# Performance work log

Measured on AMD Instinct MI355X. Metric: run time of the kernel, lower is better.

The kernel has to match this reference:

```python
import jax, jax.numpy as jnp
import numpy as np

B, N, FEAT, HID = 1024, 128, 512, 256


def setup_inputs() -> dict:
    key = jax.random.key(0)
    k1, k2, k3, k4, k5, k6 = jax.random.split(key, 6)
    x = jax.random.normal(k1, (B, FEAT), dtype=jnp.float32)
    labels = jax.random.randint(k2, (B,), 0, N, dtype=jnp.int64)
    W_proj = jax.random.normal(k3, (FEAT, HID), dtype=jnp.float32) / np.sqrt(FEAT)
    b_proj = jax.random.normal(k4, (HID,), dtype=jnp.float32) * 0.01
    means = jax.random.normal(k5, (N, HID), dtype=jnp.float32)
    # inverse covariances must be SPD so sqrt(dist_sq) is real
    A = jax.random.normal(k6, (N, HID, HID), dtype=jnp.float32)
    inv_covs = jnp.einsum('nij,nkj->nik', A, A) / HID + 0.1 * jnp.eye(HID, dtype=jnp.float32)
    return {"x": x, "labels": labels, "W_proj": W_proj, "b_proj": b_proj,
            "means": means, "inv_covs": inv_covs}


def reference(x, labels, W_proj, b_proj, means, inv_covs):
    b = x.shape[0]
    n = means.shape[0]
    x_proj = x @ W_proj + b_proj                       # (b, hid)
    delta = x_proj[:, None, :] - means[None, :, :]     # (b, n, hid)
    # batched Mahalanobis quadratic form
    dist_sq = jnp.einsum('bni,nij,bnj->bn', delta, inv_covs, delta)
    distmat = jnp.sqrt(dist_sq + 1e-12)                # (b, n)
    center_mask = (labels[:, None] == jnp.arange(n)[None, :]).astype(distmat.dtype)
    loss = jnp.clip(distmat * center_mask, 1e-12, 1e12).sum() / b
    return loss, distmat
```

## Files before the change

kernel.cpp:

```cpp
#include <hip/hip_runtime.h>
#include <hip/hip_bf16.h>

#define B_    1024
#define N_    128
#define FEAT_ 512
#define HID_  256

typedef __bf16 bf16x8 __attribute__((ext_vector_type(8)));
typedef float  f32x4  __attribute__((ext_vector_type(4)));

__device__ __forceinline__ unsigned int f2bf(float f) {
    unsigned int u = __float_as_uint(f);
    u += 0x7fffu + ((u >> 16) & 1u);
    return u >> 16;
}

__global__ __launch_bounds__(512) void prep_kernel(
    const float* __restrict__ x, const float* __restrict__ W,
    const float* __restrict__ bias, const float* __restrict__ means,
    const float* __restrict__ invcov,
    float* __restrict__ xp, unsigned short* __restrict__ xbf,
    unsigned short* __restrict__ Mbf, float* __restrict__ v2,
    float* __restrict__ cpart)
{
    __shared__ float sv[4][128];
    __shared__ float sw[2];
    const int t = threadIdx.x;
    if (blockIdx.x < 256) {
        const int n  = blockIdx.x >> 1;
        const int kh = blockIdx.x & 1;
        const int jj = t >> 7;
        const int kp = t & 127;
        const int k  = kh * 128 + kp;
        const float* Mn = invcov + (size_t)n * (HID_ * HID_);
        const float* mu = means + (size_t)n * HID_;
        unsigned short* Mb = Mbf + (size_t)n * (HID_ * HID_);
        float v = 0.f;
        #pragma unroll 8
        for (int j0 = 0; j0 < HID_; j0 += 4) {
            const int j = j0 + jj;
            const float m = Mn[(size_t)j * HID_ + k];
            v += mu[j] * m;
            const int g2 = (k >> 3) ^ ((j & 7) << 2);
            Mb[(size_t)j * HID_ + g2 * 8 + (k & 7)] = (unsigned short)f2bf(m);
        }
        sv[jj][kp] = v;
        __syncthreads();
        if (t < 128) {
            const float vk = sv[0][t] + sv[1][t] + sv[2][t] + sv[3][t];
            v2[(size_t)n * HID_ + kh * 128 + t] = 2.f * vk;
            float cc = vk * mu[kh * 128 + t];
            cc += __shfl_xor(cc, 1);
            cc += __shfl_xor(cc, 2);
            cc += __shfl_xor(cc, 4);
            cc += __shfl_xor(cc, 8);
            cc += __shfl_xor(cc, 16);
            cc += __shfl_xor(cc, 32);
            if ((t & 63) == 0) sw[t >> 6] = cc;
        }
        __syncthreads();
        if (t == 0) cpart[n * 2 + kh] = sw[0] + sw[1];
    } else {
        const int b0 = (blockIdx.x - 256) * 4;
        const int h  = t & 255;
        const int rr = t >> 8;
        const float bb = bias[h];
        float a0 = bb, a1 = bb;
        const float* x0p = x + (size_t)(b0 + rr * 2 + 0) * FEAT_;
        const float* x1p = x + (size_t)(b0 + rr * 2 + 1) * FEAT_;
        #pragma unroll 4
        for (int f = 0; f < FEAT_; f += 4) {
            const float4 xv0 = *(const float4*)(x0p + f);
            const float4 xv1 = *(const float4*)(x1p + f);
            const float w0 = W[(size_t)(f + 0) * HID_ + h];
            const float w1 = W[(size_t)(f + 1) * HID_ + h];
            const float w2 = W[(size_t)(f + 2) * HID_ + h];
            const float w3 = W[(size_t)(f + 3) * HID_ + h];
            a0 += xv0.x * w0 + xv0.y * w1 + xv0.z * w2 + xv0.w * w3;
            a1 += xv1.x * w0 + xv1.y * w1 + xv1.z * w2 + xv1.w * w3;
        }
        const int r0 = b0 + rr * 2;
        xp [(size_t)(r0 + 0) * HID_ + h] = a0;
        xp [(size_t)(r0 + 1) * HID_ + h] = a1;
        xbf[(size_t)(r0 + 0) * HID_ + h] = (unsigned short)f2bf(a0);
        xbf[(size_t)(r0 + 1) * HID_ + h] = (unsigned short)f2bf(a1);
    }
}

__global__ __launch_bounds__(512, 4) void dist_kernel(
    const float* __restrict__ xp, const unsigned short* __restrict__ xbf,
    const unsigned short* __restrict__ Mbf, const float* __restrict__ v2,
    float* __restrict__ p)
{
    extern __shared__ unsigned short Ms[];

    const int tid  = threadIdx.x;
    const int bh   = blockIdx.x;
    const int jh   = blockIdx.y;
    const int n    = blockIdx.z;
    const int wave = tid >> 6;
    const int lane = tid & 63;
    const int q    = lane >> 4;
    const int l    = lane & 15;

    const unsigned short* src = Mbf + (size_t)n * (HID_ * HID_) + (size_t)jh * 32768;
    #pragma unroll
    for (int i = 0; i < 8; ++i) {
        const int c = i * 8 + wave;
        __builtin_amdgcn_global_load_lds(
            (const __attribute__((address_space(1))) unsigned int*)(src + (size_t)c * 512 + lane * 8),
            (__attribute__((address_space(3))) unsigned int*)&Ms[c * 512],
            16, 0, 0);
    }

    bf16x8 afrag[2][8];
    #pragma unroll
    for (int rb = 0; rb < 2; ++rb) {
        const unsigned short* xr = xbf + (size_t)(bh * 256 + wave * 32 + rb * 16 + l) * HID_;
        #pragma unroll
        for (int kk = 0; kk < 8; ++kk)
            afrag[rb][kk] = *(const bf16x8*)(xr + kk * 32 + q * 8);
    }
    float v2l[8];
    #pragma unroll
    for (int ct = 0; ct < 8; ++ct)
        v2l[ct] = v2[(size_t)n * HID_ + jh * 128 + ct * 16 + l];

    __syncthreads();

    float part[8];
    #pragma unroll
    for (int i = 0; i < 8; ++i) part[i] = 0.f;

    const size_t xbase = (size_t)(bh * 256 + wave * 32 + q * 4) * HID_ + jh * 128 + l;

    #pragma unroll
    for (int ct = 0; ct < 8; ++ct) {
        float xl[8];
        #pragma unroll
        for (int rb = 0; rb < 2; ++rb)
            #pragma unroll
            for (int r = 0; r < 4; ++r)
                xl[rb * 4 + r] = xp[xbase + (size_t)(rb * 16 + r) * HID_ + ct * 16];

        f32x4 acc0 = {0.f,0.f,0.f,0.f}, acc1 = {0.f,0.f,0.f,0.f};
        #pragma unroll
        for (int kk = 0; kk < 8; ++kk) {
            const bf16x8 bfrag = *(const bf16x8*)&Ms[(ct * 16 + l) * HID_ +
                                                     (((kk * 4 + q) ^ ((l & 7) << 2)) << 3)];
            acc0 = __builtin_amdgcn_mfma_f32_16x16x32_bf16(afrag[0][kk], bfrag, acc0, 0, 0, 0);
            acc1 = __builtin_amdgcn_mfma_f32_16x16x32_bf16(afrag[1][kk], bfrag, acc1, 0, 0, 0);
        }
        const float vv = v2l[ct];
        #pragma unroll
        for (int r = 0; r < 4; ++r) {
            part[r]     += (acc0[r] - vv) * xl[r];
            part[4 + r] += (acc1[r] - vv) * xl[4 + r];
        }
    }

    #pragma unroll
    for (int i = 0; i < 8; ++i) {
        float v = part[i];
        v += __shfl_xor(v, 1);
        v += __shfl_xor(v, 2);
        v += __shfl_xor(v, 4);
        v += __shfl_xor(v, 8);
        part[i] = v;
    }
    if (l == 0) {
        float* pb = p + (size_t)jh * (B_ * N_);
        #pragma unroll
        for (int i = 0; i < 8; ++i) {
            const int row = bh * 256 + wave * 32 + (i >> 2) * 16 + q * 4 + (i & 3);
            pb[(size_t)row * N_ + n] = part[i];
        }
    }
}

__global__ __launch_bounds__(256) void finalize_kernel(
    const float* __restrict__ p, const float* __restrict__ cpart,
    float* __restrict__ out)
{
    const int i = blockIdx.x * 256 + threadIdx.x;
    const int n = i & (N_ - 1);
    const float c = cpart[n * 2] + cpart[n * 2 + 1];
    out[1 + i] = sqrtf(p[i] + p[B_ * N_ + i] + c + 1e-12f);
}

__global__ __launch_bounds__(1024) void loss_kernel(
    const float* __restrict__ distmat, const int* __restrict__ labels,
    float* __restrict__ out)
{
    __shared__ float red[16];
    const int b = threadIdx.x;
    float s = distmat[(size_t)b * N_ + labels[b]];
    #pragma unroll
    for (int m = 1; m <= 32; m <<= 1) s += __shfl_xor(s, m);
    if ((b & 63) == 0) red[b >> 6] = s;
    __syncthreads();
    if (b == 0) {
        float t = 0.f;
        #pragma unroll
        for (int i = 0; i < 16; ++i) t += red[i];
        out[0] = t / (float)B_ + (float)(N_ - 1) * 1e-12f;
    }
}

extern "C" void kernel_launch(void* const* d_in, const int* in_sizes, int n_in,
                              void* d_out, int out_size, void* d_ws, size_t ws_size,
                              hipStream_t stream) {
    const float* x      = (const float*)d_in[0];
    const int*   labels = (const int*)d_in[1];
    const float* W      = (const float*)d_in[2];
    const float* bias   = (const float*)d_in[3];
    const float* means  = (const float*)d_in[4];
    const float* invcov = (const float*)d_in[5];
    float* out = (float*)d_out;

    char* ws = (char*)d_ws;
    unsigned short* Mbf   = (unsigned short*)(ws);
    float*          xp    = (float*)         (ws + 16777216);
    unsigned short* xbf   = (unsigned short*)(ws + 17825792);
    float*          v2    = (float*)         (ws + 18350080);
    float*          cpart = (float*)         (ws + 18481152);
    float*          p     = (float*)         (ws + 18482176);

    constexpr int DIST_LDS = 128 * HID_ * 2;
    (void)hipFuncSetAttribute((const void*)dist_kernel,
                              hipFuncAttributeMaxDynamicSharedMemorySize, DIST_LDS);

    prep_kernel<<<dim3(512), 512, 0, stream>>>(x, W, bias, means, invcov,
                                               xp, xbf, Mbf, v2, cpart);
    dist_kernel<<<dim3(4, 2, N_), 512, DIST_LDS, stream>>>(xp, xbf, Mbf, v2, p);
    finalize_kernel<<<dim3((B_ * N_) / 256), 256, 0, stream>>>(p, cpart, out);
    loss_kernel<<<1, 1024, 0, stream>>>(out + 1, labels, out);
}
```

Before: 159.8 us.

## Vectorize inverse-covariance conversion with packed bf16 stores and row-wise reduction

Restructures the prep kernel so each thread loads eight consecutive floats of an inverse-covariance row and writes them as one 16-byte packed bf16 store into the swizzled layout. Before, each thread wrote a scattered 2-byte value. The mean-times-matrix product is now computed row-wise, which relies on the covariance being symmetric, and it is reduced through padded shared memory into four partial constants per class. The x projection branch now has each 256-thread block compute four rows per thread. The aim is to cut the memory-transaction overhead of streaming the 32MB covariance tensor.

```diff
diff --git a/kernel.cpp b/kernel.cpp
--- a/kernel.cpp
+++ b/kernel.cpp
@@ -14,8 +14,11 @@
     u += 0x7fffu + ((u >> 16) & 1u);
     return u >> 16;
 }
-
-__global__ __launch_bounds__(512) void prep_kernel(
+__device__ __forceinline__ unsigned int pack2(float a, float b) {
+    return f2bf(a) | (f2bf(b) << 16);
+}
+
+__global__ __launch_bounds__(256) void prep_kernel(
     const float* __restrict__ x, const float* __restrict__ W,
     const float* __restrict__ bias, const float* __restrict__ means,
     const float* __restrict__ invcov,
@@ -23,67 +26,78 @@
     unsigned short* __restrict__ Mbf, float* __restrict__ v2,
     float* __restrict__ cpart)
 {
-    __shared__ float sv[4][128];
-    __shared__ float sw[2];
     const int t = threadIdx.x;
-    if (blockIdx.x < 256) {
-        const int n  = blockIdx.x >> 1;
-        const int kh = blockIdx.x & 1;
-        const int jj = t >> 7;
-        const int kp = t & 127;
-        const int k  = kh * 128 + kp;
-        const float* Mn = invcov + (size_t)n * (HID_ * HID_);
+    if (blockIdx.x < 512) {
+        __shared__ float sv[64][33];
+        const int n  = blockIdx.x >> 2;
+        const int jq = blockIdx.x & 3;
+        const float* Mn = invcov + (size_t)n * (HID_ * HID_) + (size_t)jq * 64 * HID_;
         const float* mu = means + (size_t)n * HID_;
-        unsigned short* Mb = Mbf + (size_t)n * (HID_ * HID_);
-        float v = 0.f;
-        #pragma unroll 8
-        for (int j0 = 0; j0 < HID_; j0 += 4) {
-            const int j = j0 + jj;
-            const float m = Mn[(size_t)j * HID_ + k];
-            v += mu[j] * m;
-            const int g2 = (k >> 3) ^ ((j & 7) << 2);
-            Mb[(size_t)j * HID_ + g2 * 8 + (k & 7)] = (unsigned short)f2bf(m);
-        }
-        sv[jj][kp] = v;
+        unsigned short* Mb = Mbf + (size_t)n * (HID_ * HID_) + (size_t)jq * 64 * HID_;
+        const int gc = t & 31;
+        const int r0 = t >> 5;
+        const float4 mk0 = *(const float4*)(mu + gc * 8);
+        const float4 mk1 = *(const float4*)(mu + gc * 8 + 4);
+        #pragma unroll
+        for (int i = 0; i < 8; ++i) {
+            const int row = r0 + i * 8;
+            const float* src = Mn + (size_t)row * HID_ + gc * 8;
+            const float4 a = *(const float4*)src;
+            const float4 b = *(const float4*)(src + 4);
+            const int g2 = gc ^ ((row & 7) << 2);
+            *(uint4*)(Mb + (size_t)row * HID_ + g2 * 8) =
+                make_uint4(pack2(a.x, a.y), pack2(a.z, a.w), pack2(b.x, b.y), pack2(b.z, b.w));
+            sv[row][gc] = a.x * mk0.x + a.y * mk0.y + a.z * mk0.z + a.w * mk0.w
+                        + b.x * mk1.x + b.y * mk1.y + b.z * mk1.z + b.w * mk1.w;
+        }
         __syncthreads();
-        if (t < 128) {
-            const float vk = sv[0][t] + sv[1][t] + sv[2][t] + sv[3][t];
-            v2[(size_t)n * HID_ + kh * 128 + t] = 2.f * vk;
-            float cc = vk * mu[kh * 128 + t];
+        if (t < 64) {
+            float v = 0.f;
+            #pragma unroll
+            for (int g = 0; g < 32; ++g) v += sv[t][g];
+            const int j = jq * 64 + t;
+            v2[(size_t)n * HID_ + j] = 2.f * v;
+            float cc = v * mu[j];
             cc += __shfl_xor(cc, 1);
             cc += __shfl_xor(cc, 2);
             cc += __shfl_xor(cc, 4);
             cc += __shfl_xor(cc, 8);
             cc += __shfl_xor(cc, 16);
             cc += __shfl_xor(cc, 32);
-            if ((t & 63) == 0) sw[t >> 6] = cc;
-        }
-        __syncthreads();
-        if (t == 0) cpart[n * 2 + kh] = sw[0] + sw[1];
+            if (t == 0) cpart[n * 4 + jq] = cc;
+        }
     } else {
-        const int b0 = (blockIdx.x - 256) * 4;
-        const int h  = t & 255;
-        const int rr = t >> 8;
+        const int b0 = (blockIdx.x - 512) * 4;
+        const int h  = t;
         const float bb = bias[h];
-        float a0 = bb, a1 = bb;
-        const float* x0p = x + (size_t)(b0 + rr * 2 + 0) * FEAT_;
-        const float* x1p = x + (size_t)(b0 + rr * 2 + 1) * FEAT_;
-        #pragma unroll 4
+        float a0 = bb, a1 = bb, a2 = bb, a3 = bb;
+        const float* x0p = x + (size_t)(b0 + 0) * FEAT_;
+        const float* x1p = x + (size_t)(b0 + 1) * FEAT_;
+        const float* x2p = x + (size_t)(b0 + 2) * FEAT_;
+        const float* x3p = x + (size_t)(b0 + 3) * FEAT_;
+        #pragma unroll 2
         for (int f = 0; f < FEAT_; f += 4) {
             const float4 xv0 = *(const float4*)(x0p + f);
             const float4 xv1 = *(const float4*)(x1p + f);
+            const float4 xv2 = *(const float4*)(x2p + f);
+            const float4 xv3 = *(const float4*)(x3p + f);
             const float w0 = W[(size_t)(f + 0) * HID_ + h];
             const float w1 = W[(size_t)(f + 1) * HID_ + h];
             const float w2 = W[(size_t)(f + 2) * HID_ + h];
             const float w3 = W[(size_t)(f + 3) * HID_ + h];
             a0 += xv0.x * w0 + xv0.y * w1 + xv0.z * w2 + xv0.w * w3;
             a1 += xv1.x * w0 + xv1.y * w1 + xv1.z * w2 + xv1.w * w3;
-        }
-        const int r0 = b0 + rr * 2;
-        xp [(size_t)(r0 + 0) * HID_ + h] = a0;
-        xp [(size_t)(r0 + 1) * HID_ + h] = a1;
-        xbf[(size_t)(r0 + 0) * HID_ + h] = (unsigned short)f2bf(a0);
-        xbf[(size_t)(r0 + 1) * HID_ + h] = (unsigned short)f2bf(a1);
+            a2 += xv2.x * w0 + xv2.y * w1 + xv2.z * w2 + xv2.w * w3;
+            a3 += xv3.x * w0 + xv3.y * w1 + xv3.z * w2 + xv3.w * w3;
+        }
+        xp [(size_t)(b0 + 0) * HID_ + h] = a0;
+        xp [(size_t)(b0 + 1) * HID_ + h] = a1;
+        xp [(size_t)(b0 + 2) * HID_ + h] = a2;
+        xp [(size_t)(b0 + 3) * HID_ + h] = a3;
+        xbf[(size_t)(b0 + 0) * HID_ + h] = (unsigned short)f2bf(a0);
+        xbf[(size_t)(b0 + 1) * HID_ + h] = (unsigned short)f2bf(a1);
+        xbf[(size_t)(b0 + 2) * HID_ + h] = (unsigned short)f2bf(a2);
+        xbf[(size_t)(b0 + 3) * HID_ + h] = (unsigned short)f2bf(a3);
     }
 }
 
@@ -184,7 +198,7 @@
 {
     const int i = blockIdx.x * 256 + threadIdx.x;
     const int n = i & (N_ - 1);
-    const float c = cpart[n * 2] + cpart[n * 2 + 1];
+    const float c = cpart[n * 4] + cpart[n * 4 + 1] + cpart[n * 4 + 2] + cpart[n * 4 + 3];
     out[1 + i] = sqrtf(p[i] + p[B_ * N_ + i] + c + 1e-12f);
 }
 
@@ -224,13 +238,13 @@
     unsigned short* xbf   = (unsigned short*)(ws + 17825792);
     float*          v2    = (float*)         (ws + 18350080);
     float*          cpart = (float*)         (ws + 18481152);
-    float*          p     = (float*)         (ws + 18482176);
+    float*          p     = (float*)         (ws + 18483200);
 
     constexpr int DIST_LDS = 128 * HID_ * 2;
     (void)hipFuncSetAttribute((const void*)dist_kernel,
                               hipFuncAttributeMaxDynamicSharedMemorySize, DIST_LDS);
 
-    prep_kernel<<<dim3(512), 512, 0, stream>>>(x, W, bias, means, invcov,
+    prep_kernel<<<dim3(768), 256, 0, stream>>>(x, W, bias, means, invcov,
                                                xp, xbf, Mbf, v2, cpart);
     dist_kernel<<<dim3(4, 2, N_), 512, DIST_LDS, stream>>>(xp, xbf, Mbf, v2, p);
     finalize_kernel<<<dim3((B_ * N_) / 256), 256, 0, stream>>>(p, cpart, out);
```

Measured after the change: 147.9 us. -7.5%, faster.
